# Optimization experiments

Measured on AMD Instinct MI355X. Metric: run time of the kernel, lower is better.

Reference implementation:

```python
import jax, jax.numpy as jnp
import numpy as np

T, B, H, L = 512, 64, 1024, 2


def setup_inputs() -> dict:
    key = jax.random.key(0)
    ks = jax.random.split(key, 10)
    s = 1.0 / np.sqrt(H)  # matches init_weights uniform(-1/sqrt(H), 1/sqrt(H))
    inp = {
        "x": jax.random.normal(ks[0], (T, B, H), dtype=jnp.float32),
        "h0": jnp.zeros((L, B, H), dtype=jnp.float32),
        "Wx0": jax.random.uniform(ks[1], (3 * H, H), minval=-s, maxval=s, dtype=jnp.float32),
        "bx0": jax.random.uniform(ks[2], (3 * H,), minval=-s, maxval=s, dtype=jnp.float32),
        "Wh0": jax.random.uniform(ks[3], (3 * H, H), minval=-s, maxval=s, dtype=jnp.float32),
        "bh0": jax.random.uniform(ks[4], (3 * H,), minval=-s, maxval=s, dtype=jnp.float32),
        "Wx1": jax.random.uniform(ks[5], (3 * H, H), minval=-s, maxval=s, dtype=jnp.float32),
        "bx1": jax.random.uniform(ks[6], (3 * H,), minval=-s, maxval=s, dtype=jnp.float32),
        "Wh1": jax.random.uniform(ks[7], (3 * H, H), minval=-s, maxval=s, dtype=jnp.float32),
        "bh1": jax.random.uniform(ks[8], (3 * H,), minval=-s, maxval=s, dtype=jnp.float32),
    }
    return inp


def _gru_layer(x_seq, h0, Wx, bx, Wh, bh):
    # x_seq: [T, B, D]; precompute input-side gates for all steps (same math as per-step Linear)
    gx = jnp.einsum('tbd,gd->tbg', x_seq, Wx) + bx  # [T, B, 3H]

    def step(h, gx_t):
        gh = jnp.einsum('bh,gh->bg', h, Wh) + bh  # [B, 3H]
        rx, zx, nx = jnp.split(gx_t, 3, axis=-1)
        rh, zh, nh = jnp.split(gh, 3, axis=-1)
        r = jax.nn.sigmoid(rx + rh)
        z = jax.nn.sigmoid(zx + zh)
        n = jnp.tanh(nx + r * nh)
        h_new = (1.0 - z) * n + z * h
        return h_new, h_new

    hT, ys = jax.lax.scan(step, h0, gx)
    return ys, hT


def reference(x, h0, Wx0, bx0, Wh0, bh0, Wx1, bx1, Wh1, bh1):
    # Layer 0 (dropout=0.0 -> identity between layers)
    y0, h0_T = _gru_layer(x, h0[0], Wx0, bx0, Wh0, bh0)
    # Layer 1
    y1, h1_T = _gru_layer(y0, h0[1], Wx1, bx1, Wh1, bh1)
    h_final = jnp.stack([h0_T, h1_T], axis=0)  # [L, B, H]
    return y1, h_final
```

## Files before the change

### kernel.cpp

```cpp
#include <hip/hip_runtime.h>
#include <math.h>


#define TT 512
#define BB 64
#define HH 1024
#define NWG 256
#define NBH (BB * HH)
#define RING 32

typedef _Float16 half8 __attribute__((ext_vector_type(8)));
typedef _Float16 f16x4 __attribute__((ext_vector_type(4)));
typedef float f32x4 __attribute__((ext_vector_type(4)));
typedef unsigned int u32x4 __attribute__((ext_vector_type(4)));
typedef unsigned long long u64;

#define MFMA16 __builtin_amdgcn_mfma_f32_16x16x32_f16

__device__ inline u32x4 ldq_plain(const void* p) {
  u32x4 r; u64 a = (u64)(uintptr_t)p;
  asm volatile("global_load_dwordx4 %0, %1, off" : "=v"(r) : "v"(a));
  return r;
}
__device__ inline u32x4 ldq_agent(const void* p) {
  u32x4 r; u64 a = (u64)(uintptr_t)p;
  asm volatile("global_load_dwordx4 %0, %1, off sc0 sc1" : "=v"(r) : "v"(a));
  return r;
}
__device__ inline unsigned ldflag(const void* p) {
  unsigned r; u64 a = (u64)(uintptr_t)p;
  asm volatile("global_load_dword %0, %1, off sc0 sc1\n\ts_waitcnt vmcnt(0)"
               : "=v"(r) : "v"(a) : "memory");
  return r;
}
__device__ inline void stw(void* p, unsigned v) {
  u64 a = (u64)(uintptr_t)p;
  asm volatile("global_store_dword %0, %1, off sc0 sc1" :: "v"(a), "v"(v) : "memory");
}
__device__ inline void vdrain() { asm volatile("s_waitcnt vmcnt(0)" ::: "memory"); }

__device__ inline float fast_sigmoid(float x) { return 1.f / (1.f + __expf(-x)); }
__device__ inline float fast_tanh(float x) {
  float e = __expf(2.f * x);
  return 1.f - 2.f / (e + 1.f);
}
__device__ inline void backoff_sleep(int sl) {
  if (sl <= 0) __builtin_amdgcn_s_sleep(1);
  else if (sl == 1) __builtin_amdgcn_s_sleep(2);
  else if (sl == 2) __builtin_amdgcn_s_sleep(4);
  else __builtin_amdgcn_s_sleep(8);
}

__global__ void cvt_f32_f16_kernel(const float* __restrict__ src,
                                   _Float16* __restrict__ dst, long n) {
  long i = ((long)blockIdx.x * blockDim.x + threadIdx.x) * 4;
  long stride = (long)gridDim.x * blockDim.x * 4;
  for (long e = i; e < n; e += stride) {
    float4 v = *(const float4*)(src + e);
    f16x4 h;
    h.x = (_Float16)v.x; h.y = (_Float16)v.y;
    h.z = (_Float16)v.z; h.w = (_Float16)v.w;
    *(f16x4*)(dst + e) = h;
  }
}

__global__ void cvt_wpack_kernel(const float* __restrict__ Wh,
                                 const float* __restrict__ Wx,
                                 _Float16* __restrict__ wp) {
  int gid = blockIdx.x * 256 + threadIdx.x;
  int lane = gid & 63;
  int kst = (gid >> 6) & 63;
  int tile = gid >> 12;
  int g = tile * 16 + (lane & 15);
  int ko = (lane >> 4) * 8;
  const float* src = (kst < 32) ? (Wh + (long)g * HH + kst * 32 + ko)
                                : (Wx + (long)g * HH + (kst - 32) * 32 + ko);
  half8 h;
#pragma unroll
  for (int j = 0; j < 8; ++j) h[j] = (_Float16)src[j];
  *(half8*)(wp + (((long)tile * 64 + kst) * 64 + lane) * 8) = h;
}

__global__ void init_hf_kernel(const float* __restrict__ h0,
                               _Float16* __restrict__ h0loc,
                               _Float16* __restrict__ h1loc) {
  int i = blockIdx.x * 256 + threadIdx.x;
  float v = h0[i];
  if (i < NBH) h0loc[i] = (_Float16)v;
  else         h1loc[i - NBH] = (_Float16)v;
}

__global__ void sentinel_kernel(float* out) { out[0] = 12345.0f; }

__global__ __launch_bounds__(256, 1) void gru_persist(
    const _Float16* __restrict__ x16,
    const _Float16* __restrict__ w0p, const _Float16* __restrict__ w1p,
    const float* __restrict__ bx0, const float* __restrict__ bh0,
    const float* __restrict__ bx1, const float* __restrict__ bh1,
    const float* __restrict__ h0in,
    _Float16* __restrict__ h0loc, _Float16* __restrict__ h1loc,
    _Float16* __restrict__ hist,
    float* __restrict__ out, unsigned* __restrict__ bar)
{
  const int tid = threadIdx.x;
  const int wid = tid >> 6, lane = tid & 63;
  const int wg = blockIdx.x;
  const int lcol = lane & 15;
  const int lk = (lane >> 4) * 8;

  const int grp = wg >> 5;
  const int layer = grp >> 2;
  const int q = grp & 3;
  const int rank = wg & 31;

  __shared__ u32x4 wlds[4][6][4][64];
  __shared__ f32x4 red[4][6][64];
  __shared__ f32x4 yshare[2][64];

  unsigned* myf  = bar + grp * 1024;
  unsigned* l0if = bar + 8192 + q * 1024;
  unsigned* prog = bar + 12288 + q * 1024;

  const _Float16* wf = layer ? w1p : w0p;
  _Float16* hloc = layer ? h1loc : h0loc;
  half8 wb[6][12];
#pragma unroll
  for (int i = 0; i < 6; ++i) {
    const long tile = (long)((i >> 1) * 64 + rank * 2 + (i & 1));
#pragma unroll
    for (int ks = 0; ks < 12; ++ks)
      wb[i][ks] = *(const half8*)(wf + (tile * 64 + (wid * 16 + ks)) * 512 + lane * 8);
#pragma unroll
    for (int jj = 0; jj < 4; ++jj)
      wlds[wid][i][jj][lane] = *(const u32x4*)(wf + (tile * 64 + (wid * 16 + 12 + jj)) * 512 + lane * 8);
  }

  const int er0 = q * 16 + (lane >> 4) * 4;
  const int col = rank * 32 + wid * 16 + lcol;
  float rbv = 0.f, zbv = 0.f, nhb = 0.f, nxb = 0.f;
  float hreg[4] = {0.f, 0.f, 0.f, 0.f};
  if (wid < 2) {
    const float* bx = layer ? bx1 : bx0;
    const float* bhp = layer ? bh1 : bh0;
    rbv = bhp[col] + bx[col];
    zbv = bhp[HH + col] + bx[HH + col];
    nhb = bhp[2 * HH + col];
    nxb = bx[2 * HH + col];
#pragma unroll
    for (int j = 0; j < 4; ++j)
      hreg[j] = h0in[layer * NBH + (er0 + j) * HH + col];
  }
  __syncthreads();

  const long aoff = (long)(((q * 16 + lcol) * HH) + (wid & 1) * 512 + lk) * 2;

  int lb = 0;
  for (int t = 0; t < TT; ++t) {
    const int rd = t & 1;
    u32x4 ab[16];

    if (wid < 2) {
      if (t > 0) {
        for (;;) {
          unsigned f = ldflag(myf + lane * 16);
          if (__ballot((int)f >= t) == ~0ull) break;
          __builtin_amdgcn_s_sleep(1);
        }
        asm volatile("" ::: "memory");
      }
      const char* ap = (const char*)(hloc + (long)rd * NBH) + aoff;
#pragma unroll
      for (int ks = 0; ks < 16; ++ks) ab[ks] = ldq_agent(ap + ks * 64);
    } else if (layer == 0) {
      const char* ap = (const char*)(x16 + (long)t * NBH) + aoff;
#pragma unroll
      for (int ks = 0; ks < 16; ++ks) ab[ks] = ldq_plain(ap + ks * 64);
    } else {
      for (;;) {
        unsigned f = ldflag(l0if + (lane & 31) * 16);
        if (__ballot((int)f >= t + 1) == ~0ull) break;
        __builtin_amdgcn_s_sleep(1);
      }
      asm volatile("" ::: "memory");
      const char* ap = (const char*)(hist + (long)((t + 1) & (RING - 1)) * NBH) + aoff;
#pragma unroll
      for (int ks = 0; ks < 16; ++ks) ab[ks] = ldq_agent(ap + ks * 64);
    }
    asm volatile("s_waitcnt vmcnt(0)" ::: "memory");
    __builtin_amdgcn_sched_barrier(0);

    f32x4 acc[6] = {};
#pragma unroll
    for (int ks = 0; ks < 12; ++ks) {
      half8 a = __builtin_bit_cast(half8, ab[ks]);
#pragma unroll
      for (int i = 0; i < 6; ++i) acc[i] = MFMA16(a, wb[i][ks], acc[i], 0, 0, 0);
    }
#pragma unroll
    for (int jj = 0; jj < 4; ++jj) {
      half8 a = __builtin_bit_cast(half8, ab[12 + jj]);
#pragma unroll
      for (int i = 0; i < 6; ++i)
        acc[i] = MFMA16(a, __builtin_bit_cast(half8, wlds[wid][i][jj][lane]), acc[i], 0, 0, 0);
    }
#pragma unroll
    for (int i = 0; i < 6; ++i) red[wid][i][lane] = acc[i];
    __syncthreads();

    if (wid < 2) {
      const int h = wid;
      f32x4 rs = red[0][h][lane] + red[1][h][lane] + red[2][h][lane] + red[3][h][lane];
      f32x4 zs = red[0][2 + h][lane] + red[1][2 + h][lane] + red[2][2 + h][lane] + red[3][2 + h][lane];
      f32x4 nh = red[0][4 + h][lane] + red[1][4 + h][lane];
      f32x4 nx = red[2][4 + h][lane] + red[3][4 + h][lane];
      char* hdst = (char*)(hloc + (long)(rd ^ 1) * NBH);
      f32x4 hnv;
#pragma unroll
      for (int j = 0; j < 4; ++j) {
        const float rg = fast_sigmoid(rs[j] + rbv);
        const float zg = fast_sigmoid(zs[j] + zbv);
        const float ng = fast_tanh(nx[j] + nxb + rg * (nh[j] + nhb));
        const float hn = (1.f - zg) * ng + zg * hreg[j];
        hreg[j] = hn; hnv[j] = hn;
      }
      yshare[h][lane] = hnv;
#pragma unroll
      for (int j = 0; j < 4; ++j) {
        _Float16 hf = (_Float16)hnv[j];
        unsigned us = (unsigned)__builtin_bit_cast(unsigned short, hf);
        unsigned other = (unsigned)__shfl_xor((int)us, 1);
        if ((lane & 1) == 0)
          stw(hdst + (long)(((er0 + j) * HH) + col) * 2, us | (other << 16));
      }
      vdrain();
      if (lane == 0)
        stw(myf + (rank * 2 + wid) * 16, (unsigned)(t + 1));
    }
    __syncthreads();

    if (layer == 0) {
      if (wid == 2) {
        stw(l0if + rank * 16, (unsigned)t);
        if (t >= RING - 1) {
          const int need = t - (RING - 1);
          if (lb < need) {
            int sl = 0;
            for (;;) {
              unsigned f = ldflag(prog + (lane & 31) * 16);
              if (__ballot((int)f >= need + 16) == ~0ull) { lb = need + 16; break; }
              if (__ballot((int)f >= need) == ~0ull) { lb = need; break; }
              backoff_sleep(sl); ++sl;
            }
          }
        }
        char* rbase = (char*)(hist + (long)((t + 1) & (RING - 1)) * NBH);
#pragma unroll
        for (int h2 = 0; h2 < 2; ++h2) {
          f32x4 v = yshare[h2][lane];
          const int coln = rank * 32 + h2 * 16 + lcol;
#pragma unroll
          for (int j = 0; j < 4; ++j) {
            _Float16 hf = (_Float16)v[j];
            unsigned us = (unsigned)__builtin_bit_cast(unsigned short, hf);
            unsigned other = (unsigned)__shfl_xor((int)us, 1);
            if ((lane & 1) == 0)
              stw(rbase + (long)(((er0 + j) * HH) + coln) * 2, us | (other << 16));
          }
        }
      }
    } else {
      if (wid == 2 && lane == 0)
        stw(prog + rank * 16, (unsigned)t);
      if (wid == 3) {
        float* yo = out + (long)t * NBH;
#pragma unroll
        for (int h2 = 0; h2 < 2; ++h2) {
          f32x4 v = yshare[h2][lane];
          const int coln = rank * 32 + h2 * 16 + lcol;
#pragma unroll
          for (int j = 0; j < 4; ++j) yo[(er0 + j) * HH + coln] = v[j];
        }
      }
    }
  }

  if (layer == 0 && wid == 2) {
    vdrain();
    stw(l0if + rank * 16, (unsigned)TT);
  }
  if (wid < 2) {
#pragma unroll
    for (int j = 0; j < 4; ++j)
      out[(long)TT * NBH + (long)layer * NBH + (er0 + j) * HH + col] = hreg[j];
  }
}

extern "C" void kernel_launch(void* const* d_in, const int* in_sizes, int n_in,
                              void* d_out, int out_size, void* d_ws, size_t ws_size,
                              hipStream_t stream) {
  const float* x   = (const float*)d_in[0];
  const float* h0  = (const float*)d_in[1];
  const float* Wx0 = (const float*)d_in[2];
  const float* bx0 = (const float*)d_in[3];
  const float* Wh0 = (const float*)d_in[4];
  const float* bh0 = (const float*)d_in[5];
  const float* Wx1 = (const float*)d_in[6];
  const float* bx1 = (const float*)d_in[7];
  const float* Wh1 = (const float*)d_in[8];
  const float* bh1 = (const float*)d_in[9];
  float* out = (float*)d_out;

  const long nTBH = (long)TT * BB * HH;
  const long nWP  = (long)192 * 64 * 64 * 8;

  char* p = (char*)d_ws;
  _Float16* x16   = (_Float16*)p;  p += nTBH * 2;
  _Float16* w0p   = (_Float16*)p;  p += nWP * 2;
  _Float16* w1p   = (_Float16*)p;  p += nWP * 2;
  _Float16* hist  = (_Float16*)p;  p += (long)RING * NBH * 2;
  _Float16* h0loc = (_Float16*)p;  p += 2 * (long)NBH * 2;
  _Float16* h1loc = (_Float16*)p;  p += 2 * (long)NBH * 2;
  unsigned* bar   = (unsigned*)p;  p += 131072;
  if ((size_t)(p - (char*)d_ws) > ws_size) {
    sentinel_kernel<<<1, 1, 0, stream>>>(out);
    return;
  }

  (void)hipMemsetAsync(bar, 0, 131072, stream);
  cvt_f32_f16_kernel<<<2048, 256, 0, stream>>>(x, x16, nTBH);
  cvt_wpack_kernel<<<3072, 256, 0, stream>>>(Wh0, Wx0, w0p);
  cvt_wpack_kernel<<<3072, 256, 0, stream>>>(Wh1, Wx1, w1p);
  init_hf_kernel<<<512, 256, 0, stream>>>(h0, h0loc, h1loc);

  void* args[] = {(void*)&x16, (void*)&w0p, (void*)&w1p,
                  (void*)&bx0, (void*)&bh0, (void*)&bx1, (void*)&bh1,
                  (void*)&h0, (void*)&h0loc, (void*)&h1loc, (void*)&hist,
                  (void*)&out, (void*)&bar};
  hipError_t e = hipLaunchCooperativeKernel((const void*)gru_persist,
                                            dim3(NWG), dim3(256), args, 0, stream);
  if (e != hipSuccess) {
    gru_persist<<<NWG, 256, 0, stream>>>(x16, w0p, w1p, bx0, bh0, bx1, bh1,
                                         h0, h0loc, h1loc, hist, out, bar);
  }
}
```

Measured before the change: 2.634 ms.

## Replace per-step flag barrier with poisoned hidden-state ring polling

The per-step recurrent synchronisation is changed. The separate flag array (a drain, a flag store, then a flag poll) is replaced by a 4-slot hidden-state ring whose slots are pre-filled with a poison pattern. Consumers re-load the h tile until it contains no poison, and a spare wave re-poisons the slot two steps ahead. This removes one round-trip of flag latency per step. In exchange, every spin re-reads the full 16-vector tile, and correctness relies on stores landing at full 32-bit granularity and on 0xFFFF being a NaN that real fp16 values never take.

```diff
diff --git a/kernel.cpp b/kernel.cpp
--- a/kernel.cpp
+++ b/kernel.cpp
@@ -8,6 +8,7 @@
 #define NWG 256
 #define NBH (BB * HH)
 #define RING 32
+#define POISON 0xFFFFFFFFu
 
 typedef _Float16 half8 __attribute__((ext_vector_type(8)));
 typedef _Float16 f16x4 __attribute__((ext_vector_type(4)));
@@ -36,6 +37,10 @@
 __device__ inline void stw(void* p, unsigned v) {
   u64 a = (u64)(uintptr_t)p;
   asm volatile("global_store_dword %0, %1, off sc0 sc1" :: "v"(a), "v"(v) : "memory");
+}
+__device__ inline void stq_agent(void* p, u32x4 v) {
+  u64 a = (u64)(uintptr_t)p;
+  asm volatile("global_store_dwordx4 %0, %1, off sc0 sc1" :: "v"(a), "v"(v) : "memory");
 }
 __device__ inline void vdrain() { asm volatile("s_waitcnt vmcnt(0)" ::: "memory"); }
 
@@ -81,13 +86,17 @@
   *(half8*)(wp + (((long)tile * 64 + kst) * 64 + lane) * 8) = h;
 }
 
-__global__ void init_hf_kernel(const float* __restrict__ h0,
-                               _Float16* __restrict__ h0loc,
-                               _Float16* __restrict__ h1loc) {
+__global__ void init_ring_kernel(const float* __restrict__ h0,
+                                 _Float16* __restrict__ h0ring,
+                                 _Float16* __restrict__ h1ring) {
   int i = blockIdx.x * 256 + threadIdx.x;
-  float v = h0[i];
-  if (i < NBH) h0loc[i] = (_Float16)v;
-  else         h1loc[i - NBH] = (_Float16)v;
+  int slot = i / (2 * NBH);
+  int rem = i - slot * 2 * NBH;
+  int layer = rem / NBH;
+  int idx = rem - layer * NBH;
+  _Float16* dst = (layer ? h1ring : h0ring) + (long)slot * NBH + idx;
+  if (slot == 0) *dst = (_Float16)h0[layer * NBH + idx];
+  else *(unsigned short*)dst = 0xFFFFu;
 }
 
 __global__ void sentinel_kernel(float* out) { out[0] = 12345.0f; }
@@ -98,7 +107,7 @@
     const float* __restrict__ bx0, const float* __restrict__ bh0,
     const float* __restrict__ bx1, const float* __restrict__ bh1,
     const float* __restrict__ h0in,
-    _Float16* __restrict__ h0loc, _Float16* __restrict__ h1loc,
+    _Float16* __restrict__ h0ring, _Float16* __restrict__ h1ring,
     _Float16* __restrict__ hist,
     float* __restrict__ out, unsigned* __restrict__ bar)
 {
@@ -117,12 +126,11 @@
   __shared__ f32x4 red[4][6][64];
   __shared__ f32x4 yshare[2][64];
 
-  unsigned* myf  = bar + grp * 1024;
-  unsigned* l0if = bar + 8192 + q * 1024;
-  unsigned* prog = bar + 12288 + q * 1024;
+  unsigned* l0if = bar + q * 1024;
+  unsigned* prog = bar + 4096 + q * 1024;
 
   const _Float16* wf = layer ? w1p : w0p;
-  _Float16* hloc = layer ? h1loc : h0loc;
+  _Float16* hring = layer ? h1ring : h0ring;
   half8 wb[6][12];
 #pragma unroll
   for (int i = 0; i < 6; ++i) {
@@ -153,28 +161,35 @@
   __syncthreads();
 
   const long aoff = (long)(((q * 16 + lcol) * HH) + (wid & 1) * 512 + lk) * 2;
+  const long poff = ((long)(q * 16 + (lane >> 2)) * HH + rank * 32) * 2 + (lane & 3) * 16;
+  u32x4 pval; pval[0] = POISON; pval[1] = POISON; pval[2] = POISON; pval[3] = POISON;
 
   int lb = 0;
   for (int t = 0; t < TT; ++t) {
-    const int rd = t & 1;
     u32x4 ab[16];
 
+    if (wid == 3 && t < TT - 2)
+      stq_agent((char*)(hring + (long)((t + 2) & 3) * NBH) + poff, pval);
+
     if (wid < 2) {
-      if (t > 0) {
-        for (;;) {
-          unsigned f = ldflag(myf + lane * 16);
-          if (__ballot((int)f >= t) == ~0ull) break;
-          __builtin_amdgcn_s_sleep(1);
-        }
-        asm volatile("" ::: "memory");
-      }
-      const char* ap = (const char*)(hloc + (long)rd * NBH) + aoff;
-#pragma unroll
-      for (int ks = 0; ks < 16; ++ks) ab[ks] = ldq_agent(ap + ks * 64);
+      const char* ap = (const char*)(hring + (long)(t & 3) * NBH) + aoff;
+      for (;;) {
+#pragma unroll
+        for (int ks = 0; ks < 16; ++ks) ab[ks] = ldq_agent(ap + ks * 64);
+        asm volatile("s_waitcnt vmcnt(0)" ::: "memory");
+        bool ok = true;
+#pragma unroll
+        for (int ks = 0; ks < 16; ++ks)
+          ok = ok && (ab[ks][0] != POISON) && (ab[ks][1] != POISON)
+                  && (ab[ks][2] != POISON) && (ab[ks][3] != POISON);
+        if (__ballot(ok) == ~0ull) break;
+        __builtin_amdgcn_s_sleep(1);
+      }
     } else if (layer == 0) {
       const char* ap = (const char*)(x16 + (long)t * NBH) + aoff;
 #pragma unroll
       for (int ks = 0; ks < 16; ++ks) ab[ks] = ldq_plain(ap + ks * 64);
+      asm volatile("s_waitcnt vmcnt(0)" ::: "memory");
     } else {
       for (;;) {
         unsigned f = ldflag(l0if + (lane & 31) * 16);
@@ -185,8 +200,8 @@
       const char* ap = (const char*)(hist + (long)((t + 1) & (RING - 1)) * NBH) + aoff;
 #pragma unroll
       for (int ks = 0; ks < 16; ++ks) ab[ks] = ldq_agent(ap + ks * 64);
-    }
-    asm volatile("s_waitcnt vmcnt(0)" ::: "memory");
+      asm volatile("s_waitcnt vmcnt(0)" ::: "memory");
+    }
     __builtin_amdgcn_sched_barrier(0);
 
     f32x4 acc[6] = {};
@@ -213,7 +228,7 @@
       f32x4 zs = red[0][2 + h][lane] + red[1][2 + h][lane] + red[2][2 + h][lane] + red[3][2 + h][lane];
       f32x4 nh = red[0][4 + h][lane] + red[1][4 + h][lane];
       f32x4 nx = red[2][4 + h][lane] + red[3][4 + h][lane];
-      char* hdst = (char*)(hloc + (long)(rd ^ 1) * NBH);
+      char* hdst = (char*)(hring + (long)((t + 1) & 3) * NBH);
       f32x4 hnv;
 #pragma unroll
       for (int j = 0; j < 4; ++j) {
@@ -232,9 +247,6 @@
         if ((lane & 1) == 0)
           stw(hdst + (long)(((er0 + j) * HH) + col) * 2, us | (other << 16));
       }
-      vdrain();
-      if (lane == 0)
-        stw(myf + (rank * 2 + wid) * 16, (unsigned)(t + 1));
     }
     __syncthreads();
 
@@ -314,32 +326,32 @@
   const long nWP  = (long)192 * 64 * 64 * 8;
 
   char* p = (char*)d_ws;
-  _Float16* x16   = (_Float16*)p;  p += nTBH * 2;
-  _Float16* w0p   = (_Float16*)p;  p += nWP * 2;
-  _Float16* w1p   = (_Float16*)p;  p += nWP * 2;
-  _Float16* hist  = (_Float16*)p;  p += (long)RING * NBH * 2;
-  _Float16* h0loc = (_Float16*)p;  p += 2 * (long)NBH * 2;
-  _Float16* h1loc = (_Float16*)p;  p += 2 * (long)NBH * 2;
-  unsigned* bar   = (unsigned*)p;  p += 131072;
+  _Float16* x16    = (_Float16*)p;  p += nTBH * 2;
+  _Float16* w0p    = (_Float16*)p;  p += nWP * 2;
+  _Float16* w1p    = (_Float16*)p;  p += nWP * 2;
+  _Float16* hist   = (_Float16*)p;  p += (long)RING * NBH * 2;
+  _Float16* h0ring = (_Float16*)p;  p += 4 * (long)NBH * 2;
+  _Float16* h1ring = (_Float16*)p;  p += 4 * (long)NBH * 2;
+  unsigned* bar    = (unsigned*)p;  p += 65536;
   if ((size_t)(p - (char*)d_ws) > ws_size) {
     sentinel_kernel<<<1, 1, 0, stream>>>(out);
     return;
   }
 
-  (void)hipMemsetAsync(bar, 0, 131072, stream);
+  (void)hipMemsetAsync(bar, 0, 65536, stream);
   cvt_f32_f16_kernel<<<2048, 256, 0, stream>>>(x, x16, nTBH);
   cvt_wpack_kernel<<<3072, 256, 0, stream>>>(Wh0, Wx0, w0p);
   cvt_wpack_kernel<<<3072, 256, 0, stream>>>(Wh1, Wx1, w1p);
-  init_hf_kernel<<<512, 256, 0, stream>>>(h0, h0loc, h1loc);
+  init_ring_kernel<<<2048, 256, 0, stream>>>(h0, h0ring, h1ring);
 
   void* args[] = {(void*)&x16, (void*)&w0p, (void*)&w1p,
                   (void*)&bx0, (void*)&bh0, (void*)&bx1, (void*)&bh1,
-                  (void*)&h0, (void*)&h0loc, (void*)&h1loc, (void*)&hist,
+                  (void*)&h0, (void*)&h0ring, (void*)&h1ring, (void*)&hist,
                   (void*)&out, (void*)&bar};
   hipError_t e = hipLaunchCooperativeKernel((const void*)gru_persist,
                                             dim3(NWG), dim3(256), args, 0, stream);
   if (e != hipSuccess) {
     gru_persist<<<NWG, 256, 0, stream>>>(x16, w0p, w1p, bx0, bh0, bx1, bh1,
-                                         h0, h0loc, h1loc, hist, out, bar);
-  }
-}
+                                         h0, h0ring, h1ring, hist, out, bar);
+  }
+}
```

Result: slower. 3.121 ms (+18.5%).
